# Kernel tuning notes

Measured on AMD Instinct MI355X. Metric: run time of the kernel, lower is better.

Reference implementation:

```python
import jax, jax.numpy as jnp
from jax import lax
import numpy as np

N_NODES = 50000
N_EDGES = 800000
IN_CH = 128
HEADS = 4
OUT_CH = 32
TOP_K = 8


def setup_inputs() -> dict:
    key = jax.random.key(0)
    k1, k2, k3, k4 = jax.random.split(key, 4)
    x = jax.random.normal(k1, (N_NODES, IN_CH), jnp.float32)
    edge_index = jax.random.randint(k2, (2, N_EDGES), 0, N_NODES, dtype=jnp.int32)
    scale = float(np.sqrt(2.0 / (IN_CH + HEADS * OUT_CH)))  # xavier-ish
    W = jax.random.normal(k3, (IN_CH, HEADS * OUT_CH), jnp.float32) * scale
    att = jax.random.normal(k4, (HEADS, 2 * OUT_CH), jnp.float32) * 0.1
    return {"x": x, "W": W, "att": att, "edge_index": edge_index}


def _topk_mask_1h(e_h, row, k):
    # e_h: [E'] scores for one head; keep top-k scores within each row-segment.
    E = e_h.shape[0]
    order = jnp.lexsort((-e_h, row))          # grouped by row, descending score
    srow = row[order]
    seg_start = jnp.searchsorted(srow, srow, side="left")
    pos_in_seg = jnp.arange(E, dtype=seg_start.dtype) - seg_start
    keep_sorted = pos_in_seg < k
    return jnp.zeros((E,), jnp.bool_).at[order].set(keep_sorted)


def reference(x, W, att, edge_index):
    N = x.shape[0]
    H, C = HEADS, OUT_CH
    h = (x @ W).reshape(N, H, C)              # [N,H,C]
    # add self loops
    loops = jnp.arange(N, dtype=edge_index.dtype)
    ei = jnp.concatenate([edge_index, jnp.stack([loops, loops])], axis=1)
    row, col = ei[0], ei[1]                   # [E']
    x_i = h[row]                              # [E',H,C] gather (dst)
    x_j = h[col]                              # [E',H,C] gather (src)
    a_i, a_j = att[:, :C], att[:, C:]
    e = jnp.einsum("ehc,hc->eh", x_i, a_i) + jnp.einsum("ehc,hc->eh", x_j, a_j)
    e = jax.nn.leaky_relu(e, negative_slope=0.2)  # [E',H]
    mask = jax.vmap(lambda eh: _topk_mask_1h(eh, row, TOP_K),
                    in_axes=1, out_axes=1)(e)     # [E',H] bool
    e = jnp.where(mask, e, -jnp.inf)
    # segment softmax over rows (every node has a self loop -> non-empty segment)
    seg_max = jax.ops.segment_max(e, row, num_segments=N)
    ez = jnp.exp(e - lax.stop_gradient(seg_max)[row])  # masked edges -> 0
    denom = jax.ops.segment_sum(ez, row, num_segments=N)
    alpha = ez / denom[row]                   # [E',H]
    # dropout is identity in eval mode
    out = jax.ops.segment_sum(alpha[:, :, None] * x_j, row, num_segments=N)
    out = out.reshape(N, H * C)               # concat=True
    return jax.nn.elu(out)
```

## Files before the change

kernel.cpp:

```cpp
#include <hip/hip_runtime.h>
#include <math.h>

typedef unsigned int u32;
typedef unsigned long long u64;

#define NN 50000
#define NE 800000
#define TOPK 8
#define RSTRIDE 64
#define GTILES 782

__device__ __forceinline__ u64 shflxor64(u64 v, int m) {
    int lo = __shfl_xor((int)(u32)v, m);
    int hi = __shfl_xor((int)(u32)(v >> 32), m);
    return ((u64)(u32)hi << 32) | (u32)lo;
}

__global__ __launch_bounds__(256) void gemmdeg_k(const float* __restrict__ x,
                                                 const float* __restrict__ W,
                                                 const float* __restrict__ att,
                                                 const int* __restrict__ ei,
                                                 float* __restrict__ hbuf,
                                                 float* __restrict__ s_i,
                                                 float* __restrict__ s_j,
                                                 int* __restrict__ deg,
                                                 u32* __restrict__ ccsr) {
    __shared__ float xst[64][68];
    __shared__ float ws[64][128];
    const int t = threadIdx.x;
    const int cx = t & 15;
    const int ry = t >> 4;
    const int rbase = blockIdx.x * 64;

    const int e4 = blockIdx.x * 1024 + t * 4;
    const bool ev = e4 < NE;
    int4 er = make_int4(0, 0, 0, 0), ec = make_int4(0, 0, 0, 0);
    if (ev) {
        er = *reinterpret_cast<const int4*>(ei + e4);
        ec = *reinterpret_cast<const int4*>(ei + NE + e4);
    }
    int rk0 = RSTRIDE, rk1 = RSTRIDE, rk2 = RSTRIDE, rk3 = RSTRIDE;

    float acc[4][8];
    #pragma unroll
    for (int i = 0; i < 4; ++i)
        #pragma unroll
        for (int j = 0; j < 8; ++j) acc[i][j] = 0.f;

    for (int kk = 0; kk < 128; kk += 64) {
        if (kk) __syncthreads();
        #pragma unroll
        for (int rr = ry; rr < 64; rr += 16) {
            int gr = rbase + rr;
            float4 v = make_float4(0.f, 0.f, 0.f, 0.f);
            if (gr < NN)
                v = *reinterpret_cast<const float4*>(x + (size_t)gr * 128 + kk + cx * 4);
            xst[cx * 4 + 0][rr] = v.x;
            xst[cx * 4 + 1][rr] = v.y;
            xst[cx * 4 + 2][rr] = v.z;
            xst[cx * 4 + 3][rr] = v.w;
        }
        #pragma unroll
        for (int wk = t >> 5; wk < 64; wk += 8) {
            float4 v = *reinterpret_cast<const float4*>(W + (size_t)(kk + wk) * 128 + (t & 31) * 4);
            *reinterpret_cast<float4*>(&ws[wk][(t & 31) * 4]) = v;
        }
        __syncthreads();

        if (kk && ev) {
            rk0 = atomicAdd(deg + er.x, 1);
            rk1 = atomicAdd(deg + er.y, 1);
            rk2 = atomicAdd(deg + er.z, 1);
            rk3 = atomicAdd(deg + er.w, 1);
        }

        for (int k = 0; k < 64; ++k) {
            float4 xa = *reinterpret_cast<const float4*>(&xst[k][ry * 4]);
            float4 wa = *reinterpret_cast<const float4*>(&ws[k][cx * 8]);
            float4 wb = *reinterpret_cast<const float4*>(&ws[k][cx * 8 + 4]);
            float xv[4] = {xa.x, xa.y, xa.z, xa.w};
            float wv[8] = {wa.x, wa.y, wa.z, wa.w, wb.x, wb.y, wb.z, wb.w};
            #pragma unroll
            for (int i = 0; i < 4; ++i)
                #pragma unroll
                for (int j = 0; j < 8; ++j) acc[i][j] += xv[i] * wv[j];
        }
    }

    const int head = cx >> 2;
    float aiv[8], ajv[8];
    #pragma unroll
    for (int j = 0; j < 8; ++j) {
        aiv[j] = att[head * 64 + (cx & 3) * 8 + j];
        ajv[j] = att[head * 64 + 32 + (cx & 3) * 8 + j];
    }
    #pragma unroll
    for (int i = 0; i < 4; ++i) {
        int gr = rbase + ry * 4 + i;
        float pi = 0.f, pj = 0.f;
        #pragma unroll
        for (int j = 0; j < 8; ++j) {
            pi += acc[i][j] * aiv[j];
            pj += acc[i][j] * ajv[j];
        }
        pi += __shfl_xor(pi, 1); pi += __shfl_xor(pi, 2);
        pj += __shfl_xor(pj, 1); pj += __shfl_xor(pj, 2);
        if (gr < NN) {
            float* dst = hbuf + (size_t)gr * 128 + cx * 8;
            *reinterpret_cast<float4*>(dst)     = make_float4(acc[i][0], acc[i][1], acc[i][2], acc[i][3]);
            *reinterpret_cast<float4*>(dst + 4) = make_float4(acc[i][4], acc[i][5], acc[i][6], acc[i][7]);
            if ((cx & 3) == 0) {
                s_i[(size_t)gr * 4 + head] = pi;
                s_j[(size_t)gr * 4 + head] = pj;
            }
        }
    }

    if (ev) {
        if (rk0 < RSTRIDE) ccsr[(size_t)er.x * RSTRIDE + rk0] = (u32)ec.x;
        if (rk1 < RSTRIDE) ccsr[(size_t)er.y * RSTRIDE + rk1] = (u32)ec.y;
        if (rk2 < RSTRIDE) ccsr[(size_t)er.z * RSTRIDE + rk2] = (u32)ec.z;
        if (rk3 < RSTRIDE) ccsr[(size_t)er.w * RSTRIDE + rk3] = (u32)ec.w;
    }
}

__global__ __launch_bounds__(256) void rowsel_k(const int* __restrict__ deg,
                                                const u32* __restrict__ ccsr,
                                                const float* __restrict__ s_i,
                                                const float* __restrict__ s_j,
                                                const float* __restrict__ hbuf,
                                                float* __restrict__ out) {
    __shared__ float lal[32 * 4 * 8];
    __shared__ int   lcl[32 * 4 * 8];
    const int t = threadIdx.x;
    const int rbase = blockIdx.x * 32;
    const int lr = t >> 3;
    const int head = (t >> 1) & 3;
    const int half = t & 1;
    const int row = rbase + lr;

    u64 kl[TOPK];
    int cl[TOPK];
    #pragma unroll
    for (int i = 0; i < TOPK; ++i) { kl[i] = 0ull; cl[i] = 0; }

    int dg = 0;
    size_t o0 = (size_t)row * RSTRIDE;
    if (row < NN) {
        dg = deg[row];
        dg = (dg > RSTRIDE) ? RSTRIDE : dg;
    }

    if (half == 0 && row < NN) {
        float v = s_j[(size_t)row * 4 + head];
        u32 b = __float_as_uint(v);
        u32 fk = (b & 0x80000000u) ? ~b : (b | 0x80000000u);
        u64 key = ((u64)fk << 32) | (u32)(~(u32)(NE + row));
        kl[0] = key; cl[0] = row;
    }

    for (int j = half; j < dg; j += 2) {
        u32 col = ccsr[o0 + j];
        float v = s_j[(size_t)col * 4 + head];
        u32 b = __float_as_uint(v);
        u32 fk = (b & 0x80000000u) ? ~b : (b | 0x80000000u);
        u64 key = ((u64)fk << 32) | (u32)(~(u32)j);
        int cc = (int)col;
        #pragma unroll
        for (int i = 0; i < TOPK; ++i) {
            bool gt = key > kl[i];
            u64 tk = gt ? kl[i] : key;  kl[i] = gt ? key : kl[i];  key = tk;
            int tc = gt ? cl[i] : cc;   cl[i] = gt ? cc : cl[i];   cc = tc;
        }
    }

    u64 mk[TOPK]; int mc[TOPK];
    #pragma unroll
    for (int i = 0; i < TOPK; ++i) {
        u64 pk = shflxor64(kl[TOPK - 1 - i], 1);
        int pc = __shfl_xor(cl[TOPK - 1 - i], 1);
        bool mine = kl[i] >= pk;
        mk[i] = mine ? kl[i] : pk;
        mc[i] = mine ? cl[i] : pc;
    }
    u64 pk0 = shflxor64(kl[0], 1);
    u64 mxk = (kl[0] >= pk0) ? kl[0] : pk0;

    float si = (row < NN) ? s_i[(size_t)row * 4 + head] : 0.f;
    {
        u32 fk = (u32)(mxk >> 32);
        u32 b = (fk & 0x80000000u) ? (fk ^ 0x80000000u) : ~fk;
        float vmax = __uint_as_float(b);
        float em = si + vmax;
        float m = (em >= 0.f) ? em : 0.2f * em;
        float al[TOPK];
        float denom = 0.f;
        #pragma unroll
        for (int i = 0; i < TOPK; ++i) {
            u32 fki = (u32)(mk[i] >> 32);
            u32 bi = (fki & 0x80000000u) ? (fki ^ 0x80000000u) : ~fki;
            float v = __uint_as_float(bi);
            float e = si + v;
            e = (e >= 0.f) ? e : 0.2f * e;
            float z = (mk[i] != 0ull) ? __expf(e - m) : 0.f;
            al[i] = z;
            denom += z;
        }
        float inv = 1.f / denom;
        if (row < NN && half == 0) {
            const int base = (lr * 4 + head) * 8;
            #pragma unroll
            for (int i = 0; i < TOPK; ++i) {
                lal[base + i] = al[i] * inv;
                lcl[base + i] = mc[i];
            }
        }
    }
    __syncthreads();

    const int lane = t & 63;
    const int wid = t >> 6;
    const int q = lane >> 3;
    const int dq = lane & 7;
    for (int g = wid; g < 16; g += 4) {
        const int p = g * 8 + q;
        const int r = rbase + (p >> 2);
        const int hh = p & 3;
        if (r < NN) {
            const int base = p * 8;
            float av[8]; int cv[8];
            #pragma unroll
            for (int k = 0; k < 8; ++k) { av[k] = lal[base + k]; cv[k] = lcl[base + k]; }
            float4 a4 = make_float4(0.f, 0.f, 0.f, 0.f);
            #pragma unroll
            for (int k = 0; k < 8; ++k) {
                const float4 hv = *reinterpret_cast<const float4*>(
                    &hbuf[(size_t)cv[k] * 128 + hh * 32 + dq * 4]);
                a4.x += av[k] * hv.x;
                a4.y += av[k] * hv.y;
                a4.z += av[k] * hv.z;
                a4.w += av[k] * hv.w;
            }
            a4.x = (a4.x > 0.f) ? a4.x : expm1f(a4.x);
            a4.y = (a4.y > 0.f) ? a4.y : expm1f(a4.y);
            a4.z = (a4.z > 0.f) ? a4.z : expm1f(a4.z);
            a4.w = (a4.w > 0.f) ? a4.w : expm1f(a4.w);
            *reinterpret_cast<float4*>(&out[(size_t)r * 128 + hh * 32 + dq * 4]) = a4;
        }
    }
}

extern "C" void kernel_launch(void* const* d_in, const int* in_sizes, int n_in,
                              void* d_out, int out_size, void* d_ws, size_t ws_size,
                              hipStream_t stream) {
    const float* x   = (const float*)d_in[0];
    const float* W   = (const float*)d_in[1];
    const float* att = (const float*)d_in[2];
    const int*   ei  = (const int*)d_in[3];
    float* out = (float*)d_out;

    u32* ccsr    = (u32*)d_ws;
    float* hbuf  = (float*)(ccsr + (size_t)NN * RSTRIDE);
    float* s_i   = hbuf + 6400000;
    float* s_j   = s_i + 200000;
    int* deg     = (int*)(s_j + 200000);

    hipMemsetAsync(deg, 0, NN * sizeof(int), stream);
    gemmdeg_k<<<GTILES, 256, 0, stream>>>(x, W, att, ei, hbuf, s_i, s_j, deg, ccsr);
    rowsel_k<<<(NN + 31) / 32, 256, 0, stream>>>(deg, ccsr, s_i, s_j, hbuf, out);
}
```

Baseline: 197.3 us.

## Replace per-row global atomic CSR with bucketed edge partition and shared-memory CSR

Drops the per-edge global atomics on a 50000-entry degree array and the padded 64-wide per-row CSR. Edges are instead binned by row>>8 into 196 buckets, using block-local shared atomics and one global atomic per bucket per block. Each rowsel block then scans its bucket and builds a local CSR in shared memory, and one thread per (row, head) runs the top-k with an early-reject test, which removes the two-thread merge. This adds a kernel launch and has every bucket scanned four times, and bucket capacity (4608) or per-row capacity (64) overflow would silently drop edges.

```diff
diff --git a/kernel.cpp b/kernel.cpp
--- a/kernel.cpp
+++ b/kernel.cpp
@@ -7,24 +7,19 @@
 #define NN 50000
 #define NE 800000
 #define TOPK 8
-#define RSTRIDE 64
+#define NB 196
+#define BCAP 4608
+#define CURSTRIDE 16
 #define GTILES 782
-
-__device__ __forceinline__ u64 shflxor64(u64 v, int m) {
-    int lo = __shfl_xor((int)(u32)v, m);
-    int hi = __shfl_xor((int)(u32)(v >> 32), m);
-    return ((u64)(u32)hi << 32) | (u32)lo;
-}
-
-__global__ __launch_bounds__(256) void gemmdeg_k(const float* __restrict__ x,
-                                                 const float* __restrict__ W,
-                                                 const float* __restrict__ att,
-                                                 const int* __restrict__ ei,
-                                                 float* __restrict__ hbuf,
-                                                 float* __restrict__ s_i,
-                                                 float* __restrict__ s_j,
-                                                 int* __restrict__ deg,
-                                                 u32* __restrict__ ccsr) {
+#define PBLOCKS 391
+
+__global__ __launch_bounds__(256) void gemm_k(const float* __restrict__ x,
+                                              const float* __restrict__ W,
+                                              const float* __restrict__ att,
+                                              float* __restrict__ hbuf,
+                                              float* __restrict__ s_i,
+                                              float* __restrict__ s_j,
+                                              int* __restrict__ cursor) {
     __shared__ float xst[64][68];
     __shared__ float ws[64][128];
     const int t = threadIdx.x;
@@ -32,14 +27,7 @@
     const int ry = t >> 4;
     const int rbase = blockIdx.x * 64;
 
-    const int e4 = blockIdx.x * 1024 + t * 4;
-    const bool ev = e4 < NE;
-    int4 er = make_int4(0, 0, 0, 0), ec = make_int4(0, 0, 0, 0);
-    if (ev) {
-        er = *reinterpret_cast<const int4*>(ei + e4);
-        ec = *reinterpret_cast<const int4*>(ei + NE + e4);
-    }
-    int rk0 = RSTRIDE, rk1 = RSTRIDE, rk2 = RSTRIDE, rk3 = RSTRIDE;
+    if (blockIdx.x == 0 && t < NB) cursor[t * CURSTRIDE] = 0;
 
     float acc[4][8];
     #pragma unroll
@@ -66,13 +54,6 @@
             *reinterpret_cast<float4*>(&ws[wk][(t & 31) * 4]) = v;
         }
         __syncthreads();
-
-        if (kk && ev) {
-            rk0 = atomicAdd(deg + er.x, 1);
-            rk1 = atomicAdd(deg + er.y, 1);
-            rk2 = atomicAdd(deg + er.z, 1);
-            rk3 = atomicAdd(deg + er.w, 1);
-        }
 
         for (int k = 0; k < 64; ++k) {
             float4 xa = *reinterpret_cast<const float4*>(&xst[k][ry * 4]);
@@ -115,80 +96,120 @@
             }
         }
     }
-
+}
+
+__global__ __launch_bounds__(256) void part_k(const int* __restrict__ ei,
+                                              int* __restrict__ cursor,
+                                              u32* __restrict__ breg) {
+    __shared__ u32 cnt[NB];
+    __shared__ u32 base[NB];
+    const int t = threadIdx.x;
+    if (t < NB) cnt[t] = 0;
+    __syncthreads();
+
+    const int e0 = blockIdx.x * 2048 + t * 8;
+    const bool ev = e0 < NE;
+    int rows[8], cols[8], bk[8];
+    u32 lrk[8];
     if (ev) {
-        if (rk0 < RSTRIDE) ccsr[(size_t)er.x * RSTRIDE + rk0] = (u32)ec.x;
-        if (rk1 < RSTRIDE) ccsr[(size_t)er.y * RSTRIDE + rk1] = (u32)ec.y;
-        if (rk2 < RSTRIDE) ccsr[(size_t)er.z * RSTRIDE + rk2] = (u32)ec.z;
-        if (rk3 < RSTRIDE) ccsr[(size_t)er.w * RSTRIDE + rk3] = (u32)ec.w;
-    }
-}
-
-__global__ __launch_bounds__(256) void rowsel_k(const int* __restrict__ deg,
-                                                const u32* __restrict__ ccsr,
+        int4 ra = *reinterpret_cast<const int4*>(ei + e0);
+        int4 rb = *reinterpret_cast<const int4*>(ei + e0 + 4);
+        int4 ca = *reinterpret_cast<const int4*>(ei + NE + e0);
+        int4 cb = *reinterpret_cast<const int4*>(ei + NE + e0 + 4);
+        rows[0] = ra.x; rows[1] = ra.y; rows[2] = ra.z; rows[3] = ra.w;
+        rows[4] = rb.x; rows[5] = rb.y; rows[6] = rb.z; rows[7] = rb.w;
+        cols[0] = ca.x; cols[1] = ca.y; cols[2] = ca.z; cols[3] = ca.w;
+        cols[4] = cb.x; cols[5] = cb.y; cols[6] = cb.z; cols[7] = cb.w;
+        #pragma unroll
+        for (int i = 0; i < 8; ++i) {
+            bk[i] = rows[i] >> 8;
+            lrk[i] = atomicAdd(&cnt[bk[i]], 1u);
+        }
+    }
+    __syncthreads();
+    if (t < NB) base[t] = (cnt[t] > 0) ? (u32)atomicAdd(cursor + t * CURSTRIDE, (int)cnt[t]) : 0u;
+    __syncthreads();
+    if (ev) {
+        #pragma unroll
+        for (int i = 0; i < 8; ++i) {
+            u32 pos = base[bk[i]] + lrk[i];
+            if (pos < BCAP)
+                breg[(size_t)bk[i] * BCAP + pos] = ((u32)(rows[i] & 255) << 16) | (u32)cols[i];
+        }
+    }
+}
+
+__global__ __launch_bounds__(256) void rowsel_k(const int* __restrict__ cursor,
+                                                const u32* __restrict__ breg,
                                                 const float* __restrict__ s_i,
                                                 const float* __restrict__ s_j,
                                                 const float* __restrict__ hbuf,
                                                 float* __restrict__ out) {
-    __shared__ float lal[32 * 4 * 8];
-    __shared__ int   lcl[32 * 4 * 8];
+    __shared__ u32 lcsr[64][65];
+    __shared__ u32 ldeg[64];
+    __shared__ float lal[256 * 8];
+    __shared__ int   lcl[256 * 8];
     const int t = threadIdx.x;
-    const int rbase = blockIdx.x * 32;
-    const int lr = t >> 3;
-    const int head = (t >> 1) & 3;
-    const int half = t & 1;
-    const int row = rbase + lr;
+    const int B = blockIdx.x >> 2;
+    const int s = blockIdx.x & 3;
+    const int rbase = B * 256 + s * 64;
+
+    if (t < 64) ldeg[t] = 0;
+    __syncthreads();
+
+    int n = cursor[B * CURSTRIDE];
+    if (n > BCAP) n = BCAP;
+    const u32* reg = breg + (size_t)B * BCAP;
+    for (int i = t; i < n; i += 256) {
+        u32 e = reg[i];
+        if ((int)(e >> 22) == s) {
+            int lr = (int)((e >> 16) & 63);
+            u32 rk = atomicAdd(&ldeg[lr], 1u);
+            if (rk < 64) lcsr[lr][rk] = e & 0xFFFFu;
+        }
+    }
+    __syncthreads();
+
+    const int lrow = t >> 2;
+    const int head = t & 3;
+    const int row = rbase + lrow;
 
     u64 kl[TOPK];
     int cl[TOPK];
     #pragma unroll
     for (int i = 0; i < TOPK; ++i) { kl[i] = 0ull; cl[i] = 0; }
 
-    int dg = 0;
-    size_t o0 = (size_t)row * RSTRIDE;
+    int dgr = 0;
     if (row < NN) {
-        dg = deg[row];
-        dg = (dg > RSTRIDE) ? RSTRIDE : dg;
-    }
-
-    if (half == 0 && row < NN) {
+        dgr = (int)ldeg[lrow];
+        if (dgr > 64) dgr = 64;
         float v = s_j[(size_t)row * 4 + head];
         u32 b = __float_as_uint(v);
         u32 fk = (b & 0x80000000u) ? ~b : (b | 0x80000000u);
-        u64 key = ((u64)fk << 32) | (u32)(~(u32)(NE + row));
-        kl[0] = key; cl[0] = row;
-    }
-
-    for (int j = half; j < dg; j += 2) {
-        u32 col = ccsr[o0 + j];
+        kl[0] = ((u64)fk << 32) | (u32)(~(u32)(NE + row));
+        cl[0] = row;
+    }
+
+    for (int j = 0; j < dgr; ++j) {
+        int col = (int)lcsr[lrow][j];
         float v = s_j[(size_t)col * 4 + head];
         u32 b = __float_as_uint(v);
         u32 fk = (b & 0x80000000u) ? ~b : (b | 0x80000000u);
         u64 key = ((u64)fk << 32) | (u32)(~(u32)j);
-        int cc = (int)col;
-        #pragma unroll
-        for (int i = 0; i < TOPK; ++i) {
-            bool gt = key > kl[i];
-            u64 tk = gt ? kl[i] : key;  kl[i] = gt ? key : kl[i];  key = tk;
-            int tc = gt ? cl[i] : cc;   cl[i] = gt ? cc : cl[i];   cc = tc;
-        }
-    }
-
-    u64 mk[TOPK]; int mc[TOPK];
-    #pragma unroll
-    for (int i = 0; i < TOPK; ++i) {
-        u64 pk = shflxor64(kl[TOPK - 1 - i], 1);
-        int pc = __shfl_xor(cl[TOPK - 1 - i], 1);
-        bool mine = kl[i] >= pk;
-        mk[i] = mine ? kl[i] : pk;
-        mc[i] = mine ? cl[i] : pc;
-    }
-    u64 pk0 = shflxor64(kl[0], 1);
-    u64 mxk = (kl[0] >= pk0) ? kl[0] : pk0;
-
-    float si = (row < NN) ? s_i[(size_t)row * 4 + head] : 0.f;
+        int cc = col;
+        if (key > kl[TOPK - 1]) {
+            #pragma unroll
+            for (int i = 0; i < TOPK; ++i) {
+                bool gt = key > kl[i];
+                u64 tk = gt ? kl[i] : key;  kl[i] = gt ? key : kl[i];  key = tk;
+                int tc = gt ? cl[i] : cc;   cl[i] = gt ? cc : cl[i];   cc = tc;
+            }
+        }
+    }
+
     {
-        u32 fk = (u32)(mxk >> 32);
+        float si = (row < NN) ? s_i[(size_t)row * 4 + head] : 0.f;
+        u32 fk = (u32)(kl[0] >> 32);
         u32 b = (fk & 0x80000000u) ? (fk ^ 0x80000000u) : ~fk;
         float vmax = __uint_as_float(b);
         float em = si + vmax;
@@ -197,23 +218,20 @@
         float denom = 0.f;
         #pragma unroll
         for (int i = 0; i < TOPK; ++i) {
-            u32 fki = (u32)(mk[i] >> 32);
+            u32 fki = (u32)(kl[i] >> 32);
             u32 bi = (fki & 0x80000000u) ? (fki ^ 0x80000000u) : ~fki;
             float v = __uint_as_float(bi);
             float e = si + v;
             e = (e >= 0.f) ? e : 0.2f * e;
-            float z = (mk[i] != 0ull) ? __expf(e - m) : 0.f;
+            float z = (kl[i] != 0ull) ? __expf(e - m) : 0.f;
             al[i] = z;
             denom += z;
         }
         float inv = 1.f / denom;
-        if (row < NN && half == 0) {
-            const int base = (lr * 4 + head) * 8;
-            #pragma unroll
-            for (int i = 0; i < TOPK; ++i) {
-                lal[base + i] = al[i] * inv;
-                lcl[base + i] = mc[i];
-            }
+        #pragma unroll
+        for (int i = 0; i < TOPK; ++i) {
+            lal[t * 8 + i] = al[i] * inv;
+            lcl[t * 8 + i] = cl[i];
         }
     }
     __syncthreads();
@@ -222,7 +240,7 @@
     const int wid = t >> 6;
     const int q = lane >> 3;
     const int dq = lane & 7;
-    for (int g = wid; g < 16; g += 4) {
+    for (int g = wid; g < 32; g += 4) {
         const int p = g * 8 + q;
         const int r = rbase + (p >> 2);
         const int hh = p & 3;
@@ -259,13 +277,13 @@
     const int*   ei  = (const int*)d_in[3];
     float* out = (float*)d_out;
 
-    u32* ccsr    = (u32*)d_ws;
-    float* hbuf  = (float*)(ccsr + (size_t)NN * RSTRIDE);
+    u32* breg    = (u32*)d_ws;
+    float* hbuf  = (float*)(breg + (size_t)NB * BCAP);
     float* s_i   = hbuf + 6400000;
     float* s_j   = s_i + 200000;
-    int* deg     = (int*)(s_j + 200000);
-
-    hipMemsetAsync(deg, 0, NN * sizeof(int), stream);
-    gemmdeg_k<<<GTILES, 256, 0, stream>>>(x, W, att, ei, hbuf, s_i, s_j, deg, ccsr);
-    rowsel_k<<<(NN + 31) / 32, 256, 0, stream>>>(deg, ccsr, s_i, s_j, hbuf, out);
-}
+    int* cursor  = (int*)(s_j + 200000);
+
+    gemm_k<<<GTILES, 256, 0, stream>>>(x, W, att, hbuf, s_i, s_j, cursor);
+    part_k<<<PBLOCKS, 256, 0, stream>>>(ei, cursor, breg);
+    rowsel_k<<<NB * 4, 256, 0, stream>>>(cursor, breg, s_i, s_j, hbuf, out);
+}
```

New measurement: 173.6 us. -12.0%, faster.
